# Optimization experiments

Measured on AMD Instinct MI355X. Metric: run time of the kernel, lower is better.

## Reference

```python
import jax, jax.numpy as jnp
import numpy as np
from jax import lax

MAXHD = 200.0
MAXV = 40.0
MINA = -6.0
MAXA = 4.0
DT = 0.1
PAST = 25
NVEH = 4096
NT = 256


def setup_inputs() -> dict:
    key = jax.random.key(0)
    ks = jax.random.split(key, 8)
    s = 0.1
    return dict(
        lead_states=jax.random.uniform(ks[0], (NVEH, NT + PAST - 1, 2), dtype=jnp.float32),
        cur_states=jax.random.uniform(ks[1], (NVEH, PAST, 2), dtype=jnp.float32),
        mask=jnp.ones((NVEH, NT + PAST - 1), dtype=jnp.float32),
        conv1_w=jax.random.normal(ks[2], (3, 3, 32), dtype=jnp.float32) * s,
        conv1_b=jnp.zeros((32,), dtype=jnp.float32),
        conv2_w=jax.random.normal(ks[3], (3, 32, 64), dtype=jnp.float32) * s,
        conv2_b=jnp.zeros((64,), dtype=jnp.float32),
        dense2_w=jax.random.normal(ks[4], (384, 10), dtype=jnp.float32) * s,
        dense2_b=jnp.zeros((10,), dtype=jnp.float32),
        dense1_w=jax.random.normal(ks[5], (10, 1), dtype=jnp.float32) * s,
        dense1_b=jnp.zeros((1,), dtype=jnp.float32),
        nt=NT,
    )


def reference(lead_states, cur_states, mask, conv1_w, conv1_b, conv2_w, conv2_b,
              dense2_w, dense2_b, dense1_w, dense1_b, nt):
    nveh = lead_states.shape[0]
    lead_pos = lead_states[:, :, 0]      # (nveh, nt+past-1)
    lead_speeds = lead_states[:, :, 1]

    dn = ('NWC', 'WIO', 'NWC')

    def cnn(x):
        # x: (nveh, PAST, 3)
        x = jax.nn.relu(lax.conv_general_dilated(x, conv1_w, (1,), 'SAME', dimension_numbers=dn) + conv1_b)
        x = lax.reduce_window(x, -jnp.inf, lax.max, (1, 2, 1), (1, 2, 1), 'SAME')   # (nveh,13,32)
        x = jax.nn.relu(lax.conv_general_dilated(x, conv2_w, (1,), 'VALID', dimension_numbers=dn) + conv2_b)
        x = lax.reduce_window(x, -jnp.inf, lax.max, (1, 2, 1), (1, 2, 1), 'SAME')   # (nveh,6,64)
        x = x.reshape(x.shape[0], -1)                                               # (nveh,384)
        x = jax.nn.relu(x @ dense2_w + dense2_b)
        x = x @ dense1_w + dense1_b                                                 # (nveh,1)
        return (MAXA - MINA) * x + MINA

    def step(carry, t):
        cur_pos, cur_speeds = carry                    # each (nveh, PAST)
        lp = lax.dynamic_slice(lead_pos, (0, t), (nveh, PAST))
        ls = lax.dynamic_slice(lead_speeds, (0, t), (nveh, PAST))
        x = jnp.stack([(lp - cur_pos) / MAXHD, cur_speeds / MAXV, ls / MAXV], axis=2)
        acc = cnn(x)                                   # (nveh,1)
        pred_pos = cur_pos[:, -1:] + DT * cur_speeds[:, -1:]
        pred_sp = cur_speeds[:, -1:] + DT * acc
        new_pos = jnp.concatenate([cur_pos[:, 1:], pred_pos], axis=1)
        new_sp = jnp.concatenate([cur_speeds[:, 1:], pred_sp], axis=1)
        return (new_pos, new_sp), (pred_pos[:, 0], pred_sp[:, 0])

    init = (cur_states[:, :, 0], cur_states[:, :, 1])
    _, (pos_preds, speed_preds) = lax.scan(step, init, jnp.arange(nt))
    # (nt, nveh) -> (nveh, nt, 2)
    return jnp.stack([pos_preds.T, speed_preds.T], axis=2)
```

## Files before the change

kernel.cpp:

```cpp
#include <hip/hip_runtime.h>
#include <stdint.h>


#define PAST 25
#define NTW_MAX 280

typedef __attribute__((ext_vector_type(8))) short bf16x8;
typedef __attribute__((ext_vector_type(4))) float f32x4;
typedef unsigned short u16x2 __attribute__((ext_vector_type(2)));
#define MFMA16 __builtin_amdgcn_mfma_f32_16x16x32_bf16

static __device__ __forceinline__ uint32_t f2bf(float f) {
  union { float f; uint32_t u; } x; x.f = f;
  return (x.u + 0x7FFFu + ((x.u >> 16) & 1u)) >> 16;
}
static __device__ __forceinline__ float bf2f(uint32_t b) {
  union { uint32_t u; float f; } x; x.u = b << 16; return x.f;
}
static __device__ __forceinline__ uint32_t pkbf(float lo, float hi) {
  uint32_t r;
  asm("v_cvt_pk_bf16_f32 %0, %1, %2" : "=v"(r) : "v"(lo), "v"(hi));
  return r;
}
static __device__ __forceinline__ f32x4 bcast4(float v) { f32x4 r = {v, v, v, v}; return r; }

static __device__ __forceinline__ uint32_t pkmax(uint32_t a, uint32_t b) {
#if __has_builtin(__builtin_elementwise_max)
  union U { uint32_t w; u16x2 v; } x, y; x.w = a; y.w = b;
  x.v = __builtin_elementwise_max(x.v, y.v);
  return x.w;
#else
  uint32_t al = a << 16, bl = b << 16;
  uint32_t lo = (al > bl ? al : bl) >> 16;
  uint32_t ah = a & 0xffff0000u, bh = b & 0xffff0000u;
  uint32_t hi = ah > bh ? ah : bh;
  return lo | hi;
#endif
}
static __device__ __forceinline__ uint4 maxq(uint4 a, uint4 b) {
  uint4 r; r.x = pkmax(a.x, b.x); r.y = pkmax(a.y, b.y);
  r.z = pkmax(a.z, b.z); r.w = pkmax(a.w, b.w); return r;
}
static __device__ __forceinline__ int w21(int x) { if (x >= 21) x -= 21; if (x >= 21) x -= 21; return x; }
static __device__ __forceinline__ int w17(int x) { if (x >= 17) x -= 17; if (x >= 17) x -= 17; return x; }
static __device__ __forceinline__ void lds_fence() {
  asm volatile("s_waitcnt lgkmcnt(0)" ::: "memory");
}
static __device__ __forceinline__ float rsum16(float x) {
  x += __builtin_bit_cast(float, __builtin_amdgcn_update_dpp(0, __builtin_bit_cast(int, x), 0x121, 0xf, 0xf, true));
  x += __builtin_bit_cast(float, __builtin_amdgcn_update_dpp(0, __builtin_bit_cast(int, x), 0x122, 0xf, 0xf, true));
  x += __builtin_bit_cast(float, __builtin_amdgcn_update_dpp(0, __builtin_bit_cast(int, x), 0x124, 0xf, 0xf, true));
  x += __builtin_bit_cast(float, __builtin_amdgcn_update_dpp(0, __builtin_bit_cast(int, x), 0x128, 0xf, 0xf, true));
  return x;
}

union FragU { bf16x8 v; uint16_t u[8]; uint4 q; };
struct RowD { f32x4 d0, d1; };

struct __align__(16) SMem {
  uint32_t Xcol[8][33][2];
  float2 lead[8][NTW_MAX];
  uint16_t P[24 * 8 * 32];
  uint16_t O2[20 * 8 * 64];
  float2 obuf[2][8][64];
  f32x4 JpartA[2][64];
  f32x4 JpartB[2][64];
};

__global__ __launch_bounds__(256, 2) void rnncf_kernel(
    const float* __restrict__ lead_states, const float* __restrict__ cur_states,
    const float* __restrict__ conv1_w, const float* __restrict__ conv1_b,
    const float* __restrict__ conv2_w, const float* __restrict__ conv2_b,
    const float* __restrict__ dense2_w, const float* __restrict__ dense2_b,
    const float* __restrict__ dense1_w, const float* __restrict__ dense1_b,
    float* __restrict__ out, int nt, int ntw) {
  __shared__ SMem sm;
  const int tid = threadIdx.x;
  const int lane = tid & 63;
  const int wid = tid >> 6;
  const int n = lane & 15;
  const int quad = lane >> 4;
  const int vbase = blockIdx.x * 8;
  const int bpidx = ((lane >> 4) << 6) | ((lane & 7) << 2);

  if (tid < 200) {
    int v = tid & 7, u = tid >> 3;
    const float2 l = *(const float2*)(lead_states + ((size_t)(vbase + v) * ntw + u) * 2);
    const float2 c = *(const float2*)(cur_states + ((size_t)(vbase + v) * PAST + u) * 2);
    float x0 = (l.x - c.x) * 0.005f;
    uint32_t w0 = pkbf(x0, c.y * 0.025f);
    sm.Xcol[v][u][0] = w0;
    sm.Xcol[v][u][1] = pkbf(l.y * 0.025f, x0 - bf2f(w0 & 0xffffu));
  }
#pragma unroll
  for (int v = 0; v < 8; ++v)
    for (int i = tid; i < ntw; i += 256)
      sm.lead[v][i] = *(const float2*)(lead_states + ((size_t)(vbase + v) * ntw + i) * 2);

  float pos_s = 0.f, spd_s = 0.f;
  if (wid == 3 && quad < 2 && n < 4) {
    int veh = quad * 4 + n;
    const float2 c = *(const float2*)(cur_states + ((size_t)(vbase + veh) * PAST + 24) * 2);
    pos_s = c.x * 0.005f; spd_s = c.y * 0.025f;
  }

  FragU B1[2];
#pragma unroll
  for (int ct = 0; ct < 2; ++ct)
#pragma unroll
    for (int jj = 0; jj < 8; ++jj) {
      int k = quad * 8 + jj;
      int dw = k & 3, cig = (k >> 2) & 3;
      float w = 0.f;
      if (k < 16 && dw < 3) {
        int ci = (cig == 3) ? 0 : cig;
        w = conv1_w[(dw * 3 + ci) * 32 + ct * 16 + n];
      }
      B1[ct].u[jj] = (uint16_t)f2bf(w);
    }
  FragU B2[3][4];
#pragma unroll
  for (int dw = 0; dw < 3; ++dw)
#pragma unroll
    for (int ct = 0; ct < 4; ++ct)
#pragma unroll
      for (int jj = 0; jj < 8; ++jj) {
        int kap = quad * 8 + jj;
        int ci = (kap & 1) * 16 + (kap >> 1);
        B2[dw][ct].u[jj] = (uint16_t)f2bf(conv2_w[(dw * 32 + ci) * 64 + ct * 16 + n]);
      }
  FragU Bd[12];
#pragma unroll
  for (int kt = 0; kt < 12; ++kt)
#pragma unroll
    for (int jj = 0; jj < 8; ++jj) {
      int flat = kt * 32 + quad * 8 + jj;
      int jp = flat >> 6, kap = flat & 63;
      int co = (kap & 3) * 16 + (kap >> 2);
      Bd[kt].u[jj] = (uint16_t)f2bf((n < 10) ? dense2_w[(jp * 64 + co) * 10 + n] : 0.f);
    }
  f32x4 b1q0, b1q1;
#pragma unroll
  for (int r = 0; r < 4; ++r) {
    b1q0[r] = conv1_b[quad * 4 + r];
    b1q1[r] = conv1_b[16 + quad * 4 + r];
  }
  float b2v[4];
#pragma unroll
  for (int ct = 0; ct < 4; ++ct) b2v[ct] = conv2_b[ct * 16 + n];
  const float d2bv = (n < 10) ? dense2_b[n] : 0.f;
  const float wd1v = (n < 10) ? dense1_w[n] : 0.f;
  const float bd1v = dense1_b[0];

  auto pIdx = [&](int s, int veh, int ch) { return ((s * 8 + veh) * 4 + ch) * 8; };
  auto oIdx = [&](int s, int veh, int ch) { return ((s * 8 + veh) * 8 + ch) * 8; };

  auto build_x = [&](int c, int padL, int padR) -> FragU {
    int h = quad & 1, v8 = n & 7;
    uint32_t d0 = padL ? 0u : sm.Xcol[v8][(c - 1) & 31][h];
    uint32_t d1 = sm.Xcol[v8][c & 31][h];
    uint32_t d2 = padR ? 0u : sm.Xcol[v8][(c + 1) & 31][h];
    FragU a;
    a.q.x = __builtin_amdgcn_perm(d1, d0, 0x05040100u);
    a.q.y = d2 & 0xffffu;
    a.q.z = __builtin_amdgcn_perm(d1, d0, 0x07060302u);
    a.q.w = d2 >> 16;
    return a;
  };

  auto conv1s_row = [&](int c, int padL, int padR) -> RowD {
    FragU a = build_x(c, padL, padR);
    RowD rd;
    rd.d0 = MFMA16(B1[0].v, a.v, b1q0, 0, 0, 0);
    rd.d1 = MFMA16(B1[1].v, a.v, b1q1, 0, 0, 0);
    return rd;
  };

  auto relumax4 = [&](const f32x4& a, const f32x4& b) -> f32x4 {
    f32x4 r;
#pragma unroll
    for (int i = 0; i < 4; ++i) r[i] = fmaxf(fmaxf(a[i], b[i]), 0.f);
    return r;
  };
  auto relu4 = [&](const f32x4& a) -> f32x4 {
    f32x4 r;
#pragma unroll
    for (int i = 0; i < 4; ++i) r[i] = fmaxf(a[i], 0.f);
    return r;
  };
  auto pack4 = [&](const f32x4& p0, const f32x4& p1) -> uint4 {
    uint4 w;
    w.x = pkbf(p0[0], p1[0]); w.y = pkbf(p0[1], p1[1]);
    w.z = pkbf(p0[2], p1[2]); w.w = pkbf(p0[3], p1[3]);
    return w;
  };
  auto p_store = [&](const uint4& w, int ds) {
    if (n < 8) *(uint4*)&sm.P[pIdx(ds, n, quad ^ (n & 3))] = w;
  };
  auto pool_store = [&](const RowD& A, const RowD& Bq, int ds) {
    p_store(pack4(relumax4(A.d0, Bq.d0), relumax4(A.d1, Bq.d1)), ds);
  };
  auto bperm_frag = [&](const uint4& w) -> FragU {
    FragU f;
    f.q.x = (uint32_t)__builtin_amdgcn_ds_bpermute(bpidx, (int)w.x);
    f.q.y = (uint32_t)__builtin_amdgcn_ds_bpermute(bpidx, (int)w.y);
    f.q.z = (uint32_t)__builtin_amdgcn_ds_bpermute(bpidx, (int)w.z);
    f.q.w = (uint32_t)__builtin_amdgcn_ds_bpermute(bpidx, (int)w.w);
    return f;
  };

  auto ld_P = [&](int s) -> FragU {
    FragU a; a.q = *(const uint4*)&sm.P[pIdx(s, n & 7, quad ^ (n & 3))]; return a;
  };

  auto conv2_acc = [&](f32x4* acc, int slot, int dw) {
    FragU a = ld_P(slot);
#pragma unroll
    for (int ct = 0; ct < 4; ++ct) acc[ct] = MFMA16(a.v, B2[dw][ct].v, acc[ct], 0, 0, 0);
  };

  auto conv2_accf = [&](f32x4* acc, const FragU& a, int dw) {
#pragma unroll
    for (int ct = 0; ct < 4; ++ct) acc[ct] = MFMA16(a.v, B2[dw][ct].v, acc[ct], 0, 0, 0);
  };

  auto o2_write = [&](const f32x4* acc, int ds) {
    if (quad < 2) {
#pragma unroll
      for (int r = 0; r < 4; ++r) {
        int veh = quad * 4 + r;
        float m0 = fmaxf(acc[0][r], 0.f), m1 = fmaxf(acc[1][r], 0.f);
        float m2 = fmaxf(acc[2][r], 0.f), m3 = fmaxf(acc[3][r], 0.f);
        uint2 w2; w2.x = pkbf(m0, m1); w2.y = pkbf(m2, m3);
        *(uint2*)&sm.O2[oIdx(ds, veh, (n >> 1) ^ (veh & 7)) + (n & 1) * 4] = w2;
      }
    }
  };

  auto dense_jp = [&](int pa, int pb, int jp, f32x4& a0, f32x4& a1) {
#pragma unroll
    for (int hf = 0; hf < 2; ++hf) {
      uint4 qa = *(const uint4*)&sm.O2[oIdx(pa, n & 7, (hf * 4 + quad) ^ (n & 7))];
      if (pb >= 0) {
        uint4 qb = *(const uint4*)&sm.O2[oIdx(pb, n & 7, (hf * 4 + quad) ^ (n & 7))];
        qa = maxq(qa, qb);
      }
      FragU a; a.q = qa;
      if (hf == 0) a0 = MFMA16(a.v, Bd[jp * 2].v, a0, 0, 0, 0);
      else         a1 = MFMA16(a.v, Bd[jp * 2 + 1].v, a1, 0, 0, 0);
    }
  };

  auto dense_jp_pre = [&](int pa, const uint4* qpre, int jp, f32x4& a0, f32x4& a1) {
#pragma unroll
    for (int hf = 0; hf < 2; ++hf) {
      uint4 qa = *(const uint4*)&sm.O2[oIdx(pa, n & 7, (hf * 4 + quad) ^ (n & 7))];
      if (qpre) qa = maxq(qa, qpre[hf]);
      FragU a; a.q = qa;
      if (hf == 0) a0 = MFMA16(a.v, Bd[jp * 2].v, a0, 0, 0, 0);
      else         a1 = MFMA16(a.v, Bd[jp * 2 + 1].v, a1, 0, 0, 0);
    }
  };

  auto flush_out = [&](int bi, int t0, int cnt) {
    int vv = lane >> 3;
    int s0 = (lane & 7) * 8;
#pragma unroll
    for (int k = 0; k < 8; ++k) {
      int s = s0 + k;
      if (s < cnt) {
        float2 d = sm.obuf[bi][vv][s];
        *(float2*)(out + ((size_t)(vbase + vv) * nt + t0 + s) * 2) = d;
      }
    }
  };

  __syncthreads();

#pragma unroll
  for (int i = 0; i < 5; ++i) {
    int g = 2 + wid + 4 * i;
    RowD A = conv1s_row(g, 0, 0);
    RowD Bq = conv1s_row(g + 1, 0, 0);
    pool_store(A, Bq, g % 21);
  }
  __syncthreads();

#pragma unroll
  for (int i = 0; i < 4; ++i) {
    int a = 2 + wid + 4 * i;
    f32x4 acc[4];
#pragma unroll
    for (int ct = 0; ct < 4; ++ct) acc[ct] = bcast4(b2v[ct]);
    conv2_acc(acc, a % 21, 0);
    conv2_acc(acc, (a + 2) % 21, 1);
    conv2_acc(acc, (a + 4) % 21, 2);
    o2_write(acc, a % 17);
  }
  __syncthreads();

  RowD c1A = {};
  f32x4 accA[4] = {}, accB[4] = {};
  if (wid == 1) {
    RowD A = conv1s_row(0, 1, 0), Bq = conv1s_row(1, 0, 0);
    pool_store(A, Bq, 23);
    lds_fence();
    f32x4 aj[4];
#pragma unroll
    for (int ct = 0; ct < 4; ++ct) aj[ct] = bcast4(b2v[ct]);
    conv2_acc(aj, 23, 0); conv2_acc(aj, 2, 1); conv2_acc(aj, 4, 2);
    o2_write(aj, 17);
  } else if (wid == 2) {
    RowD A = conv1s_row(1, 1, 0), Bq = conv1s_row(2, 0, 0);
    pool_store(A, Bq, 1);
    lds_fence();
    f32x4 aj[4];
#pragma unroll
    for (int ct = 0; ct < 4; ++ct) aj[ct] = bcast4(b2v[ct]);
    conv2_acc(aj, 1, 0); conv2_acc(aj, 3, 1); conv2_acc(aj, 5, 2);
    o2_write(aj, 18);
  } else if (wid == 0) {
    RowD A = conv1s_row(2, 1, 0), Bq = conv1s_row(3, 0, 0);
    pool_store(A, Bq, 21);
  } else {
#pragma unroll
    for (int ct = 0; ct < 4; ++ct) accA[ct] = bcast4(b2v[ct]);
    conv2_acc(accA, 18, 0);
    conv2_acc(accA, 20, 1);
#pragma unroll
    for (int ct = 0; ct < 4; ++ct) accB[ct] = bcast4(b2v[ct]);
    conv2_acc(accB, 20, 0);
    c1A = conv1s_row(22, 0, 0);
  }
  __syncthreads();

  if (wid == 0) {
    f32x4 a0 = bcast4(d2bv), a1 = bcast4(0.f);
    dense_jp(17, 2, 0, a0, a1);
    dense_jp(4, 6, 1, a0, a1);
    dense_jp(8, 10, 2, a0, a1);
    dense_jp(12, 14, 3, a0, a1);
    sm.JpartA[0][lane] = a0;
    sm.JpartB[0][lane] = a1;
  }
  __syncthreads();

  if (wid == 3) __builtin_amdgcn_s_setprio(2);

  int tm21 = 0, tm17 = 0;
  for (int t = 0; t < nt; ++t) {
    const int sP22 = w21(tm21 + 22);
    const int sO16 = w17(tm17 + 16), sO18 = w17(tm17 + 18);
    const int tm21n = (tm21 + 1 == 21) ? 0 : tm21 + 1;
    const int tm17n = (tm17 + 1 == 17) ? 0 : tm17 + 1;
    const int sP18n = w21(tm21n + 18), sP20n = w21(tm21n + 20);

    if (wid == 3) {
      f32x4 jpA = sm.JpartA[t & 1][lane];
      f32x4 jpB = sm.JpartB[t & 1][lane];
      uint4 qj8[2];
#pragma unroll
      for (int hf = 0; hf < 2; ++hf)
        qj8[hf] = *(const uint4*)&sm.O2[oIdx(sO16, n & 7, (hf * 4 + quad) ^ (n & 7))];
      FragU fA18 = ld_P(sP18n);
      FragU fA20 = ld_P(sP20n);
      RowD Bq = conv1s_row(t + 23, 0, 0);
      RowD Sg = conv1s_row(t + 24, 0, 1);
      uint4 w11 = pack4(relumax4(c1A.d0, Bq.d0), relumax4(c1A.d1, Bq.d1));
      uint4 w12 = pack4(relu4(Sg.d0), relu4(Sg.d1));
      p_store(w11, sP22);
      c1A = Bq;
      FragU f11 = bperm_frag(w11);
      FragU f12 = bperm_frag(w12);
      conv2_accf(accA, f11, 2);
      conv2_accf(accB, f11, 1);
      conv2_accf(accB, f12, 2);
      o2_write(accA, sO18);
      o2_write(accB, 19);
      f32x4 acc2 = bcast4(0.f), acc3 = bcast4(0.f);
      f32x4 acc4 = bcast4(0.f), acc5 = bcast4(0.f);
      dense_jp_pre(sO18, qj8, 4, acc2, acc3);
      dense_jp_pre(19, (const uint4*)nullptr, 5, acc4, acc5);
      float s0 = fmaxf(jpA[0] + jpB[0] + acc2[0] + acc3[0] + acc4[0] + acc5[0], 0.f) * wd1v;
      float s1 = fmaxf(jpA[1] + jpB[1] + acc2[1] + acc3[1] + acc4[1] + acc5[1], 0.f) * wd1v;
      float s2 = fmaxf(jpA[2] + jpB[2] + acc2[2] + acc3[2] + acc4[2] + acc5[2], 0.f) * wd1v;
      float s3 = fmaxf(jpA[3] + jpB[3] + acc2[3] + acc3[3] + acc4[3] + acc5[3], 0.f) * wd1v;
      s0 = rsum16(s0); s1 = rsum16(s1); s2 = rsum16(s2); s3 = rsum16(s3);
      if (quad < 2 && n < 4) {
        int veh = quad * 4 + n;
        float sv = (n == 0) ? s0 : (n == 1) ? s1 : (n == 2) ? s2 : s3;
        float accv = 10.f * (sv + bd1v) - 6.f;
        float np_s = pos_s + 0.02f * spd_s;
        float nsp = spd_s * 40.f + 0.1f * accv;
        pos_s = np_s; spd_s = nsp * 0.025f;
        float2 o2v; o2v.x = np_s * 200.f; o2v.y = nsp;
        sm.obuf[(t >> 6) & 1][veh][t & 63] = o2v;
        int ui = t + PAST; if (ui > ntw - 1) ui = ntw - 1;
        float2 ln = sm.lead[veh][ui];
        float x0 = ln.x * 0.005f - np_s;
        uint32_t wlo = pkbf(x0, spd_s);
        sm.Xcol[veh][(t + PAST) & 31][0] = wlo;
        sm.Xcol[veh][(t + PAST) & 31][1] = pkbf(ln.y * 0.025f, x0 - bf2f(wlo & 0xffffu));
      }
#pragma unroll
      for (int ct = 0; ct < 4; ++ct) accA[ct] = bcast4(b2v[ct]);
      conv2_accf(accA, fA18, 0);
      conv2_accf(accA, fA20, 1);
#pragma unroll
      for (int ct = 0; ct < 4; ++ct) accB[ct] = bcast4(b2v[ct]);
      conv2_accf(accB, fA20, 0);
    } else if (wid == 0) {
      f32x4 a0 = bcast4(d2bv), a1 = bcast4(0.f);
      dense_jp(17 + ((t + 1) & 1), w17(tm17n + 2), 0, a0, a1);
      dense_jp(w17(tm17n + 4), w17(tm17n + 6), 1, a0, a1);
      dense_jp(w17(tm17n + 8), w17(tm17n + 10), 2, a0, a1);
      dense_jp(w17(tm17n + 12), w17(tm17n + 14), 3, a0, a1);
      sm.JpartA[(t + 1) & 1][lane] = a0;
      sm.JpartB[(t + 1) & 1][lane] = a1;
    } else if (wid == 1) {
      if ((t & 63) == 0 && t > 0) flush_out(((t >> 6) & 1) ^ 1, t - 64, 64);
      f32x4 aj[4];
#pragma unroll
      for (int ct = 0; ct < 4; ++ct) aj[ct] = bcast4(b2v[ct]);
      conv2_acc(aj, (t & 1) ? 23 : 21, 0);
      conv2_acc(aj, w21(tm21 + 4), 1);
      conv2_acc(aj, w21(tm21 + 6), 2);
      o2_write(aj, 17 + (t & 1));
    } else {
      RowD A = conv1s_row(t + 3, 1, 0);
      RowD Bq = conv1s_row(t + 4, 0, 0);
      pool_store(A, Bq, (t & 1) ? 21 : 23);
    }
    __syncthreads();

    tm21 = tm21n; tm17 = tm17n;
  }

  if (wid == 1) {
    int t0 = (nt - 1) & ~63;
    flush_out(((nt - 1) >> 6) & 1, t0, nt - t0);
  }
}

extern "C" void kernel_launch(void* const* d_in, const int* in_sizes, int n_in,
                              void* d_out, int out_size, void* d_ws, size_t ws_size,
                              hipStream_t stream) {
  const float* lead = (const float*)d_in[0];
  const float* cur  = (const float*)d_in[1];
  const float* c1w = (const float*)d_in[3];
  const float* c1b = (const float*)d_in[4];
  const float* c2w = (const float*)d_in[5];
  const float* c2b = (const float*)d_in[6];
  const float* d2w = (const float*)d_in[7];
  const float* d2b = (const float*)d_in[8];
  const float* d1w = (const float*)d_in[9];
  const float* d1b = (const float*)d_in[10];
  float* out = (float*)d_out;

  int nveh = in_sizes[1] / (PAST * 2);
  int ntw  = in_sizes[2] / nveh;
  int nt   = ntw - PAST + 1;
  int nblocks = nveh / 8;

  rnncf_kernel<<<nblocks, 256, 0, stream>>>(lead, cur, c1w, c1b, c2w, c2b,
                                            d2w, d2b, d1w, d1b, out, nt, ntw);
}
```

Baseline: 400.5 us.

## Process two timesteps per barrier with deeper producer pipeline and compact lead storage

The recurrent loop now advances two timesteps per __syncthreads, so each producer wave (conv1, conv2, dense partials) runs two steps ahead into 4-deep ring buffers, while the critical wave 3 does two sequential steps. The prologue is rebuilt to prefill the deeper pipeline. Lead states are stored as fp32 position plus prescaled bf16 speed, and the output buffer is halved. This halves barrier count on the serial critical path but adds LDS ring slots and register pressure, and it assumes nt is even.

```diff
diff --git a/kernel.cpp b/kernel.cpp
--- a/kernel.cpp
+++ b/kernel.cpp
@@ -43,9 +43,6 @@
 }
 static __device__ __forceinline__ int w21(int x) { if (x >= 21) x -= 21; if (x >= 21) x -= 21; return x; }
 static __device__ __forceinline__ int w17(int x) { if (x >= 17) x -= 17; if (x >= 17) x -= 17; return x; }
-static __device__ __forceinline__ void lds_fence() {
-  asm volatile("s_waitcnt lgkmcnt(0)" ::: "memory");
-}
 static __device__ __forceinline__ float rsum16(float x) {
   x += __builtin_bit_cast(float, __builtin_amdgcn_update_dpp(0, __builtin_bit_cast(int, x), 0x121, 0xf, 0xf, true));
   x += __builtin_bit_cast(float, __builtin_amdgcn_update_dpp(0, __builtin_bit_cast(int, x), 0x122, 0xf, 0xf, true));
@@ -59,12 +56,13 @@
 
 struct __align__(16) SMem {
   uint32_t Xcol[8][33][2];
-  float2 lead[8][NTW_MAX];
-  uint16_t P[24 * 8 * 32];
-  uint16_t O2[20 * 8 * 64];
-  float2 obuf[2][8][64];
-  f32x4 JpartA[2][64];
-  f32x4 JpartB[2][64];
+  float    leadx[8][256];
+  uint16_t leady[8][256];
+  uint16_t P[25 * 8 * 32];
+  uint16_t O2[22 * 8 * 64];
+  float2 obuf[2][8][32];
+  f32x4 JpartA[4][64];
+  f32x4 JpartB[4][64];
 };
 
 __global__ __launch_bounds__(256, 2) void rnncf_kernel(
@@ -94,8 +92,11 @@
   }
 #pragma unroll
   for (int v = 0; v < 8; ++v)
-    for (int i = tid; i < ntw; i += 256)
-      sm.lead[v][i] = *(const float2*)(lead_states + ((size_t)(vbase + v) * ntw + i) * 2);
+    for (int i = 25 + tid; i < ntw; i += 256) {
+      const float2 l = *(const float2*)(lead_states + ((size_t)(vbase + v) * ntw + i) * 2);
+      sm.leadx[v][i - 25] = l.x;
+      sm.leady[v][i - 25] = (uint16_t)f2bf(l.y * 0.025f);
+    }
 
   float pos_s = 0.f, spd_s = 0.f;
   if (wid == 3 && quad < 2 && n < 4) {
@@ -264,10 +265,10 @@
 
   auto flush_out = [&](int bi, int t0, int cnt) {
     int vv = lane >> 3;
-    int s0 = (lane & 7) * 8;
-#pragma unroll
-    for (int k = 0; k < 8; ++k) {
-      int s = s0 + k;
+    int s0 = (lane & 7) * 4;
+#pragma unroll
+    for (int kk = 0; kk < 4; ++kk) {
+      int s = s0 + kk;
       if (s < cnt) {
         float2 d = sm.obuf[bi][vv][s];
         *(float2*)(out + ((size_t)(vbase + vv) * nt + t0 + s) * 2) = d;
@@ -301,144 +302,194 @@
 
   RowD c1A = {};
   f32x4 accA[4] = {}, accB[4] = {};
-  if (wid == 1) {
+  if (wid == 0) {
     RowD A = conv1s_row(0, 1, 0), Bq = conv1s_row(1, 0, 0);
     pool_store(A, Bq, 23);
-    lds_fence();
+  } else if (wid == 1) {
+    RowD A = conv1s_row(1, 1, 0), Bq = conv1s_row(2, 0, 0);
+    pool_store(A, Bq, 24);
+  }
+  __syncthreads();
+  if (wid == 0) {
     f32x4 aj[4];
 #pragma unroll
     for (int ct = 0; ct < 4; ++ct) aj[ct] = bcast4(b2v[ct]);
     conv2_acc(aj, 23, 0); conv2_acc(aj, 2, 1); conv2_acc(aj, 4, 2);
     o2_write(aj, 17);
+  } else if (wid == 1) {
+    f32x4 aj[4];
+#pragma unroll
+    for (int ct = 0; ct < 4; ++ct) aj[ct] = bcast4(b2v[ct]);
+    conv2_acc(aj, 24, 0); conv2_acc(aj, 3, 1); conv2_acc(aj, 5, 2);
+    o2_write(aj, 18);
   } else if (wid == 2) {
-    RowD A = conv1s_row(1, 1, 0), Bq = conv1s_row(2, 0, 0);
-    pool_store(A, Bq, 1);
-    lds_fence();
-    f32x4 aj[4];
-#pragma unroll
-    for (int ct = 0; ct < 4; ++ct) aj[ct] = bcast4(b2v[ct]);
-    conv2_acc(aj, 1, 0); conv2_acc(aj, 3, 1); conv2_acc(aj, 5, 2);
-    o2_write(aj, 18);
-  } else if (wid == 0) {
-    RowD A = conv1s_row(2, 1, 0), Bq = conv1s_row(3, 0, 0);
+    RowD A = conv1s_row(4, 1, 0), Bq = conv1s_row(5, 0, 0);
     pool_store(A, Bq, 21);
   } else {
-#pragma unroll
-    for (int ct = 0; ct < 4; ++ct) accA[ct] = bcast4(b2v[ct]);
-    conv2_acc(accA, 18, 0);
-    conv2_acc(accA, 20, 1);
-#pragma unroll
-    for (int ct = 0; ct < 4; ++ct) accB[ct] = bcast4(b2v[ct]);
-    conv2_acc(accB, 20, 0);
-    c1A = conv1s_row(22, 0, 0);
-  }
-  __syncthreads();
-
+    RowD A = conv1s_row(5, 1, 0), Bq = conv1s_row(6, 0, 0);
+    pool_store(A, Bq, 22);
+  }
+  __syncthreads();
   if (wid == 0) {
     f32x4 a0 = bcast4(d2bv), a1 = bcast4(0.f);
     dense_jp(17, 2, 0, a0, a1);
     dense_jp(4, 6, 1, a0, a1);
     dense_jp(8, 10, 2, a0, a1);
     dense_jp(12, 14, 3, a0, a1);
-    sm.JpartA[0][lane] = a0;
-    sm.JpartB[0][lane] = a1;
+    sm.JpartA[0][lane] = a0; sm.JpartB[0][lane] = a1;
+  } else if (wid == 1) {
+    f32x4 a0 = bcast4(d2bv), a1 = bcast4(0.f);
+    dense_jp(18, 3, 0, a0, a1);
+    dense_jp(5, 7, 1, a0, a1);
+    dense_jp(9, 11, 2, a0, a1);
+    dense_jp(13, 15, 3, a0, a1);
+    sm.JpartA[1][lane] = a0; sm.JpartB[1][lane] = a1;
+  } else if (wid == 2) {
+    RowD A = conv1s_row(2, 1, 0), Bq = conv1s_row(3, 0, 0);
+    pool_store(A, Bq, 23);
+  } else {
+    RowD A = conv1s_row(3, 1, 0), Bq = conv1s_row(4, 0, 0);
+    pool_store(A, Bq, 24);
+  }
+  __syncthreads();
+  if (wid == 0) {
+    f32x4 aj[4];
+#pragma unroll
+    for (int ct = 0; ct < 4; ++ct) aj[ct] = bcast4(b2v[ct]);
+    conv2_acc(aj, 23, 0); conv2_acc(aj, 4, 1); conv2_acc(aj, 6, 2);
+    o2_write(aj, 19);
+  } else if (wid == 1) {
+    f32x4 aj[4];
+#pragma unroll
+    for (int ct = 0; ct < 4; ++ct) aj[ct] = bcast4(b2v[ct]);
+    conv2_acc(aj, 24, 0); conv2_acc(aj, 5, 1); conv2_acc(aj, 7, 2);
+    o2_write(aj, 20);
+  } else if (wid == 3) {
+#pragma unroll
+    for (int ct = 0; ct < 4; ++ct) accA[ct] = bcast4(b2v[ct]);
+    conv2_acc(accA, 18, 0);
+    conv2_acc(accA, 20, 1);
+#pragma unroll
+    for (int ct = 0; ct < 4; ++ct) accB[ct] = bcast4(b2v[ct]);
+    conv2_acc(accB, 20, 0);
+    c1A = conv1s_row(22, 0, 0);
   }
   __syncthreads();
 
   if (wid == 3) __builtin_amdgcn_s_setprio(2);
 
-  int tm21 = 0, tm17 = 0;
-  for (int t = 0; t < nt; ++t) {
-    const int sP22 = w21(tm21 + 22);
-    const int sO16 = w17(tm17 + 16), sO18 = w17(tm17 + 18);
-    const int tm21n = (tm21 + 1 == 21) ? 0 : tm21 + 1;
-    const int tm17n = (tm17 + 1 == 17) ? 0 : tm17 + 1;
-    const int sP18n = w21(tm21n + 18), sP20n = w21(tm21n + 20);
-
+  int tmA21 = 0, tmA17 = 0;
+  const int nsup = nt >> 1;
+  for (int k = 0; k < nsup; ++k) {
     if (wid == 3) {
-      f32x4 jpA = sm.JpartA[t & 1][lane];
-      f32x4 jpB = sm.JpartB[t & 1][lane];
-      uint4 qj8[2];
-#pragma unroll
-      for (int hf = 0; hf < 2; ++hf)
-        qj8[hf] = *(const uint4*)&sm.O2[oIdx(sO16, n & 7, (hf * 4 + quad) ^ (n & 7))];
-      FragU fA18 = ld_P(sP18n);
-      FragU fA20 = ld_P(sP20n);
-      RowD Bq = conv1s_row(t + 23, 0, 0);
-      RowD Sg = conv1s_row(t + 24, 0, 1);
-      uint4 w11 = pack4(relumax4(c1A.d0, Bq.d0), relumax4(c1A.d1, Bq.d1));
-      uint4 w12 = pack4(relu4(Sg.d0), relu4(Sg.d1));
-      p_store(w11, sP22);
-      c1A = Bq;
-      FragU f11 = bperm_frag(w11);
-      FragU f12 = bperm_frag(w12);
-      conv2_accf(accA, f11, 2);
-      conv2_accf(accB, f11, 1);
-      conv2_accf(accB, f12, 2);
-      o2_write(accA, sO18);
-      o2_write(accB, 19);
-      f32x4 acc2 = bcast4(0.f), acc3 = bcast4(0.f);
-      f32x4 acc4 = bcast4(0.f), acc5 = bcast4(0.f);
-      dense_jp_pre(sO18, qj8, 4, acc2, acc3);
-      dense_jp_pre(19, (const uint4*)nullptr, 5, acc4, acc5);
-      float s0 = fmaxf(jpA[0] + jpB[0] + acc2[0] + acc3[0] + acc4[0] + acc5[0], 0.f) * wd1v;
-      float s1 = fmaxf(jpA[1] + jpB[1] + acc2[1] + acc3[1] + acc4[1] + acc5[1], 0.f) * wd1v;
-      float s2 = fmaxf(jpA[2] + jpB[2] + acc2[2] + acc3[2] + acc4[2] + acc5[2], 0.f) * wd1v;
-      float s3 = fmaxf(jpA[3] + jpB[3] + acc2[3] + acc3[3] + acc4[3] + acc5[3], 0.f) * wd1v;
-      s0 = rsum16(s0); s1 = rsum16(s1); s2 = rsum16(s2); s3 = rsum16(s3);
-      if (quad < 2 && n < 4) {
-        int veh = quad * 4 + n;
-        float sv = (n == 0) ? s0 : (n == 1) ? s1 : (n == 2) ? s2 : s3;
-        float accv = 10.f * (sv + bd1v) - 6.f;
-        float np_s = pos_s + 0.02f * spd_s;
-        float nsp = spd_s * 40.f + 0.1f * accv;
-        pos_s = np_s; spd_s = nsp * 0.025f;
-        float2 o2v; o2v.x = np_s * 200.f; o2v.y = nsp;
-        sm.obuf[(t >> 6) & 1][veh][t & 63] = o2v;
-        int ui = t + PAST; if (ui > ntw - 1) ui = ntw - 1;
-        float2 ln = sm.lead[veh][ui];
-        float x0 = ln.x * 0.005f - np_s;
-        uint32_t wlo = pkbf(x0, spd_s);
-        sm.Xcol[veh][(t + PAST) & 31][0] = wlo;
-        sm.Xcol[veh][(t + PAST) & 31][1] = pkbf(ln.y * 0.025f, x0 - bf2f(wlo & 0xffffu));
-      }
-#pragma unroll
-      for (int ct = 0; ct < 4; ++ct) accA[ct] = bcast4(b2v[ct]);
-      conv2_accf(accA, fA18, 0);
-      conv2_accf(accA, fA20, 1);
-#pragma unroll
-      for (int ct = 0; ct < 4; ++ct) accB[ct] = bcast4(b2v[ct]);
-      conv2_accf(accB, fA20, 0);
+#pragma unroll
+      for (int d = 0; d < 2; ++d) {
+        const int t = 2 * k + d;
+        const int sP22 = w21(tmA21 + d + 22);
+        const int sO16 = w17(tmA17 + d + 16);
+        const int sO18 = w17(tmA17 + d + 18);
+        const int sP18n = w21(tmA21 + d + 19);
+        const int sP20n = w21(tmA21 + d + 21);
+        f32x4 jpA = sm.JpartA[t & 3][lane];
+        f32x4 jpB = sm.JpartB[t & 3][lane];
+        uint4 qj8[2];
+#pragma unroll
+        for (int hf = 0; hf < 2; ++hf)
+          qj8[hf] = *(const uint4*)&sm.O2[oIdx(sO16, n & 7, (hf * 4 + quad) ^ (n & 7))];
+        FragU fA18 = ld_P(sP18n);
+        FragU fA20 = ld_P(sP20n);
+        RowD Bq = conv1s_row(t + 23, 0, 0);
+        RowD Sg = conv1s_row(t + 24, 0, 1);
+        uint4 w11 = pack4(relumax4(c1A.d0, Bq.d0), relumax4(c1A.d1, Bq.d1));
+        uint4 w12 = pack4(relu4(Sg.d0), relu4(Sg.d1));
+        p_store(w11, sP22);
+        c1A = Bq;
+        FragU f11 = bperm_frag(w11);
+        FragU f12 = bperm_frag(w12);
+        conv2_accf(accA, f11, 2);
+        conv2_accf(accB, f11, 1);
+        conv2_accf(accB, f12, 2);
+        o2_write(accA, sO18);
+        o2_write(accB, 21);
+        f32x4 acc2 = bcast4(0.f), acc3 = bcast4(0.f);
+        f32x4 acc4 = bcast4(0.f), acc5 = bcast4(0.f);
+        dense_jp_pre(sO18, qj8, 4, acc2, acc3);
+        dense_jp_pre(21, (const uint4*)nullptr, 5, acc4, acc5);
+        float s0 = fmaxf(jpA[0] + jpB[0] + acc2[0] + acc3[0] + acc4[0] + acc5[0], 0.f) * wd1v;
+        float s1 = fmaxf(jpA[1] + jpB[1] + acc2[1] + acc3[1] + acc4[1] + acc5[1], 0.f) * wd1v;
+        float s2 = fmaxf(jpA[2] + jpB[2] + acc2[2] + acc3[2] + acc4[2] + acc5[2], 0.f) * wd1v;
+        float s3 = fmaxf(jpA[3] + jpB[3] + acc2[3] + acc3[3] + acc4[3] + acc5[3], 0.f) * wd1v;
+        s0 = rsum16(s0); s1 = rsum16(s1); s2 = rsum16(s2); s3 = rsum16(s3);
+        if (quad < 2 && n < 4) {
+          int veh = quad * 4 + n;
+          float sv = (n == 0) ? s0 : (n == 1) ? s1 : (n == 2) ? s2 : s3;
+          float accv = 10.f * (sv + bd1v) - 6.f;
+          float np_s = pos_s + 0.02f * spd_s;
+          float nsp = spd_s * 40.f + 0.1f * accv;
+          pos_s = np_s; spd_s = nsp * 0.025f;
+          float2 o2v; o2v.x = np_s * 200.f; o2v.y = nsp;
+          sm.obuf[(t >> 5) & 1][veh][t & 31] = o2v;
+          int li = t; if (li > ntw - 26) li = ntw - 26;
+          float lnx = sm.leadx[veh][li];
+          float lny = bf2f(sm.leady[veh][li]);
+          float x0 = lnx * 0.005f - np_s;
+          uint32_t wlo = pkbf(x0, spd_s);
+          sm.Xcol[veh][(t + PAST) & 31][0] = wlo;
+          sm.Xcol[veh][(t + PAST) & 31][1] = pkbf(lny, x0 - bf2f(wlo & 0xffffu));
+        }
+#pragma unroll
+        for (int ct = 0; ct < 4; ++ct) accA[ct] = bcast4(b2v[ct]);
+        conv2_accf(accA, fA18, 0);
+        conv2_accf(accA, fA20, 1);
+#pragma unroll
+        for (int ct = 0; ct < 4; ++ct) accB[ct] = bcast4(b2v[ct]);
+        conv2_accf(accB, fA20, 0);
+      }
     } else if (wid == 0) {
-      f32x4 a0 = bcast4(d2bv), a1 = bcast4(0.f);
-      dense_jp(17 + ((t + 1) & 1), w17(tm17n + 2), 0, a0, a1);
-      dense_jp(w17(tm17n + 4), w17(tm17n + 6), 1, a0, a1);
-      dense_jp(w17(tm17n + 8), w17(tm17n + 10), 2, a0, a1);
-      dense_jp(w17(tm17n + 12), w17(tm17n + 14), 3, a0, a1);
-      sm.JpartA[(t + 1) & 1][lane] = a0;
-      sm.JpartB[(t + 1) & 1][lane] = a1;
+#pragma unroll
+      for (int e = 0; e < 2; ++e) {
+        const int tau = 2 * k + 2 + e;
+        f32x4 a0 = bcast4(d2bv), a1 = bcast4(0.f);
+        dense_jp(17 + (tau & 3), w17(tmA17 + 4 + e), 0, a0, a1);
+        dense_jp(w17(tmA17 + 6 + e), w17(tmA17 + 8 + e), 1, a0, a1);
+        dense_jp(w17(tmA17 + 10 + e), w17(tmA17 + 12 + e), 2, a0, a1);
+        dense_jp(w17(tmA17 + 14 + e), w17(tmA17 + 16 + e), 3, a0, a1);
+        sm.JpartA[tau & 3][lane] = a0;
+        sm.JpartB[tau & 3][lane] = a1;
+      }
     } else if (wid == 1) {
-      if ((t & 63) == 0 && t > 0) flush_out(((t >> 6) & 1) ^ 1, t - 64, 64);
-      f32x4 aj[4];
-#pragma unroll
-      for (int ct = 0; ct < 4; ++ct) aj[ct] = bcast4(b2v[ct]);
-      conv2_acc(aj, (t & 1) ? 23 : 21, 0);
-      conv2_acc(aj, w21(tm21 + 4), 1);
-      conv2_acc(aj, w21(tm21 + 6), 2);
-      o2_write(aj, 17 + (t & 1));
+      if ((k & 15) == 0 && k > 0) {
+        int t0 = 2 * k - 32;
+        flush_out((t0 >> 5) & 1, t0, 32);
+      }
+#pragma unroll
+      for (int e = 0; e < 2; ++e) {
+        const int tau = 2 * k + 4 + e;
+        f32x4 aj[4];
+#pragma unroll
+        for (int ct = 0; ct < 4; ++ct) aj[ct] = bcast4(b2v[ct]);
+        conv2_acc(aj, 21 + (tau & 3), 0);
+        conv2_acc(aj, w21(tmA21 + 6 + e), 1);
+        conv2_acc(aj, w21(tmA21 + 8 + e), 2);
+        o2_write(aj, 17 + (tau & 3));
+      }
     } else {
-      RowD A = conv1s_row(t + 3, 1, 0);
-      RowD Bq = conv1s_row(t + 4, 0, 0);
-      pool_store(A, Bq, (t & 1) ? 21 : 23);
+#pragma unroll
+      for (int f = 0; f < 2; ++f) {
+        const int tau = 2 * k + 6 + f;
+        RowD A = conv1s_row(tau, 1, 0);
+        RowD Bq = conv1s_row(tau + 1, 0, 0);
+        pool_store(A, Bq, 21 + (tau & 3));
+      }
     }
     __syncthreads();
-
-    tm21 = tm21n; tm17 = tm17n;
+    tmA21 = w21(tmA21 + 2);
+    tmA17 = w17(tmA17 + 2);
   }
 
   if (wid == 1) {
-    int t0 = (nt - 1) & ~63;
-    flush_out(((nt - 1) >> 6) & 1, t0, nt - t0);
+    int t0 = (nt - 1) & ~31;
+    flush_out((t0 >> 5) & 1, t0, nt - t0);
   }
 }
 
```

Result: faster. 390.2 us (-2.6%).
